# Kernel optimization log

Measured on AMD Instinct MI355X. Metric: run time of the kernel, lower is better.

The kernel has to match this reference:

```python
import jax, jax.numpy as jnp
import numpy as np

WIDTH = 2048
HEIGHT = 2048
N_SAMPLES = 4194304


def setup_inputs() -> dict:
    key = jax.random.key(0)
    k_uv, k_tex = jax.random.split(key)
    # uvs in [0,1) -> after (uv+1)/2 maps to [0.5,1), always in-range texel coords
    uvs = jax.random.uniform(k_uv, (N_SAMPLES, 2), dtype=jnp.float32)
    texture = jax.random.normal(k_tex, (WIDTH, HEIGHT, 3), dtype=jnp.float32)
    return {"uvs": uvs, "texture": texture}


def reference(uvs, texture):
    W, H = texture.shape[0], texture.shape[1]
    # map [-1,1] -> [0, dim-1] texel coordinates
    u = (uvs[:, 0] + 1.0) * 0.5 * (W - 1)
    v = (uvs[:, 1] + 1.0) * 0.5 * (H - 1)
    u0 = jnp.floor(u).astype(jnp.int32)
    u1 = jnp.ceil(u).astype(jnp.int32)
    v0 = jnp.floor(v).astype(jnp.int32)
    v1 = jnp.ceil(v).astype(jnp.int32)
    a = (u - u0.astype(jnp.float32))[:, None]  # [N,1]
    b = (v - v0.astype(jnp.float32))[:, None]  # [N,1]
    # 4-corner gather + weighted combine (exact weights from the torch source)
    colors = (texture[u0, v0] * a + texture[u1, v0] * (1.0 - a)) * b \
           + (texture[u0, v1] * a + texture[u1, v1] * (1.0 - a)) * (1.0 - b)
    return colors  # [N,3]
```

## Files before the change

### kernel.cpp

```cpp
#include <hip/hip_runtime.h>

#define TEX_W 2048
#define TEX_H 2048

__global__ __launch_bounds__(256) void difftex_bilinear_kernel(
    const float* __restrict__ uvs,
    const float* __restrict__ tex,
    float* __restrict__ out,
    int n)
{
    int i = blockIdx.x * blockDim.x + threadIdx.x;
    if (i >= n) return;

    float2 uv = reinterpret_cast<const float2*>(uvs)[i];

    float u = (uv.x + 1.0f) * 0.5f * (float)(TEX_W - 1);
    float v = (uv.y + 1.0f) * 0.5f * (float)(TEX_H - 1);

    float fu0 = floorf(u);
    float fv0 = floorf(v);
    int u0 = (int)fu0;
    int v0 = (int)fv0;
    int u1 = (int)ceilf(u);
    int v1 = (int)ceilf(v);

    float a = u - fu0;
    float b = v - fv0;
    float ia = 1.0f - a;
    float ib = 1.0f - b;

    const float* r0 = tex + u0 * (TEX_H * 3);
    const float* r1 = tex + u1 * (TEX_H * 3);
    int c0 = v0 * 3;
    int c1 = v1 * 3;

    float t00x = r0[c0 + 0], t00y = r0[c0 + 1], t00z = r0[c0 + 2];
    float t10x = r1[c0 + 0], t10y = r1[c0 + 1], t10z = r1[c0 + 2];
    float t01x = r0[c1 + 0], t01y = r0[c1 + 1], t01z = r0[c1 + 2];
    float t11x = r1[c1 + 0], t11y = r1[c1 + 1], t11z = r1[c1 + 2];

    float ox = (t00x * a + t10x * ia) * b + (t01x * a + t11x * ia) * ib;
    float oy = (t00y * a + t10y * ia) * b + (t01y * a + t11y * ia) * ib;
    float oz = (t00z * a + t10z * ia) * b + (t01z * a + t11z * ia) * ib;

    out[i * 3 + 0] = ox;
    out[i * 3 + 1] = oy;
    out[i * 3 + 2] = oz;
}

extern "C" void kernel_launch(void* const* d_in, const int* in_sizes, int n_in,
                              void* d_out, int out_size, void* d_ws, size_t ws_size,
                              hipStream_t stream) {
    const float* uvs = (const float*)d_in[0];
    const float* tex = (const float*)d_in[1];
    float* out = (float*)d_out;

    int n = in_sizes[0] / 2;
    int block = 256;
    int grid = (n + block - 1) / block;
    difftex_bilinear_kernel<<<grid, block, 0, stream>>>(uvs, tex, out, n);
}
```

Baseline: 221.7 us.

## Repack RGB texture to padded RGBA in workspace and gather with float4 loads

Adds a pre-pass kernel that converts the packed RGB float texture into a 16-byte-per-texel RGBA layout in the workspace. The bilinear kernel then fetches each corner with a single aligned float4 load instead of three scalar loads. This aims to cut the number of memory instructions and transactions in the random gather. The cost is a full texture read and a larger write on every call. It falls back to the scalar kernel if the workspace is too small.

```diff
diff --git a/kernel.cpp b/kernel.cpp
--- a/kernel.cpp
+++ b/kernel.cpp
@@ -2,8 +2,69 @@
 
 #define TEX_W 2048
 #define TEX_H 2048
+#define N_TEXELS (TEX_W * TEX_H)
+#define RGBA_BYTES ((size_t)N_TEXELS * 16)
 
-__global__ __launch_bounds__(256) void difftex_bilinear_kernel(
+__global__ __launch_bounds__(256) void dtx_repack(
+    const float4* __restrict__ src,
+    float4* __restrict__ dst,
+    int quads)
+{
+    int t = blockIdx.x * blockDim.x + threadIdx.x;
+    if (t >= quads) return;
+    float4 s0 = src[3 * t + 0];
+    float4 s1 = src[3 * t + 1];
+    float4 s2 = src[3 * t + 2];
+    dst[4 * t + 0] = make_float4(s0.x, s0.y, s0.z, 0.0f);
+    dst[4 * t + 1] = make_float4(s0.w, s1.x, s1.y, 0.0f);
+    dst[4 * t + 2] = make_float4(s1.z, s1.w, s2.x, 0.0f);
+    dst[4 * t + 3] = make_float4(s2.y, s2.z, s2.w, 0.0f);
+}
+
+__global__ __launch_bounds__(256) void dtx_gather(
+    const float* __restrict__ uvs,
+    const float4* __restrict__ texq,
+    float* __restrict__ out,
+    int n)
+{
+    int i = blockIdx.x * blockDim.x + threadIdx.x;
+    if (i >= n) return;
+
+    float2 uv = reinterpret_cast<const float2*>(uvs)[i];
+
+    float u = (uv.x + 1.0f) * 0.5f * (float)(TEX_W - 1);
+    float v = (uv.y + 1.0f) * 0.5f * (float)(TEX_H - 1);
+
+    float fu0 = floorf(u);
+    float fv0 = floorf(v);
+    int u0 = (int)fu0;
+    int v0 = (int)fv0;
+    int u1 = (int)ceilf(u);
+    int v1 = (int)ceilf(v);
+
+    float a = u - fu0;
+    float b = v - fv0;
+    float ia = 1.0f - a;
+    float ib = 1.0f - b;
+
+    int r0 = u0 * TEX_H;
+    int r1 = u1 * TEX_H;
+
+    float4 t00 = texq[r0 + v0];
+    float4 t10 = texq[r1 + v0];
+    float4 t01 = texq[r0 + v1];
+    float4 t11 = texq[r1 + v1];
+
+    float ox = (t00.x * a + t10.x * ia) * b + (t01.x * a + t11.x * ia) * ib;
+    float oy = (t00.y * a + t10.y * ia) * b + (t01.y * a + t11.y * ia) * ib;
+    float oz = (t00.z * a + t10.z * ia) * b + (t01.z * a + t11.z * ia) * ib;
+
+    out[i * 3 + 0] = ox;
+    out[i * 3 + 1] = oy;
+    out[i * 3 + 2] = oz;
+}
+
+__global__ __launch_bounds__(256) void dtx_scalar(
     const float* __restrict__ uvs,
     const float* __restrict__ tex,
     float* __restrict__ out,
@@ -58,5 +119,15 @@
     int n = in_sizes[0] / 2;
     int block = 256;
     int grid = (n + block - 1) / block;
-    difftex_bilinear_kernel<<<grid, block, 0, stream>>>(uvs, tex, out, n);
+
+    if (ws_size >= RGBA_BYTES) {
+        int quads = N_TEXELS / 4;
+        int pk_grid = (quads + block - 1) / block;
+        dtx_repack<<<pk_grid, block, 0, stream>>>(
+            (const float4*)tex, (float4*)d_ws, quads);
+        dtx_gather<<<grid, block, 0, stream>>>(
+            uvs, (const float4*)d_ws, out, n);
+    } else {
+        dtx_scalar<<<grid, block, 0, stream>>>(uvs, tex, out, n);
+    }
 }
```

New measurement: 261.1 us. 1.18x slower.
